# Optimization experiments

Measured on AMD Instinct MI355X. Metric: run time of the kernel, lower is better.

The kernel has to match this reference:

```python
import jax, jax.numpy as jnp
import numpy as np

LN_EPS = 1e-5  # torch.nn.LayerNorm default

QLEN, MLEN, BATCH, D_MODEL = 1024, 1024, 8, 1024


def _ft_matrix(qlen, klen):
    """Real part of the causal Fourier matrix (imag part never contributes:
    the input is real and the module takes .real of the product)."""
    ft_len = klen - qlen + 1
    m = jnp.arange(qlen, dtype=jnp.float32)
    k = jnp.arange(ft_len, dtype=jnp.float32)
    base = jnp.cos((2.0 * float(np.pi)) * jnp.outer(m, k) / float(ft_len))
    base = base / float(np.sqrt(ft_len))                      # [qlen, ft_len]
    mat = jnp.pad(base, ((0, 0), (klen - ft_len, 0)))          # left-pad -> [qlen, klen]
    # row i rolled left by (qlen - 1 - i), vectorized as a gather
    shift = (qlen - 1) - jnp.arange(qlen)                      # [qlen]
    cols = (jnp.arange(klen)[None, :] + shift[:, None]) % klen  # [qlen, klen]
    mat = jnp.take_along_axis(mat, cols, axis=1)
    rows = jnp.arange(qlen)[:, None]
    js = jnp.arange(klen)[None, :]
    # tril(diagonal=klen-qlen) AND triu(0)  (same_length=True)
    mask = (js <= rows + (klen - qlen)) & (js >= rows)
    return jnp.where(mask, mat, jnp.float32(0.0))


def setup_inputs() -> dict:
    key = jax.random.key(0)
    k1, k2, k3 = jax.random.split(key, 3)
    return {
        "dec_inp": jax.random.normal(k1, (QLEN, BATCH, D_MODEL), dtype=jnp.float32),
        "pos_emb": jax.random.normal(k2, (QLEN + MLEN, 1, D_MODEL), dtype=jnp.float32),
        "mems": jax.random.normal(k3, (MLEN, BATCH, D_MODEL), dtype=jnp.float32),
        "gamma": jnp.ones((D_MODEL,), dtype=jnp.float32),
        "beta": jnp.zeros((D_MODEL,), dtype=jnp.float32),
        "add_position": 1,
    }


def reference(dec_inp, pos_emb, mems, gamma, beta, add_position):
    qlen = dec_inp.shape[0]
    klen = qlen + mems.shape[0]
    cat = jnp.concatenate([mems, dec_inp], axis=0)  # [klen, b, d]
    if add_position:
        cat = cat + pos_emb  # dropout is identity in eval mode
    ft_mat = _ft_matrix(qlen, klen)                 # [qlen, klen]
    ft = jnp.einsum('ml,lbd->mbd', ft_mat, cat)     # real part of complex matmul
    x = dec_inp + ft / float(np.sqrt(klen))
    mu = jnp.mean(x, axis=-1, keepdims=True)
    var = jnp.var(x, axis=-1, keepdims=True)
    return gamma * (x - mu) * jax.lax.rsqrt(var + LN_EPS) + beta
```

## Files before the change

kernel.cpp:

```cpp
#include <hip/hip_runtime.h>
#include <hip/hip_bf16.h>

#define QLEN   1024
#define MLEN   1024
#define KLEN   2048
#define BATCH  8
#define DMODEL 1024
#define NCOLS  (BATCH * DMODEL)
#define FTLEN  1025

#define BM 128
#define BN 256
#define BK 64
#define NT 18

typedef __attribute__((ext_vector_type(4))) float f32x4;
typedef __attribute__((ext_vector_type(8))) short bf16x8;

typedef __attribute__((address_space(1))) const unsigned int as1_u32;
typedef __attribute__((address_space(3))) unsigned int as3_u32;

static __device__ __forceinline__ unsigned short f2bf(float f) {
    unsigned int u = __builtin_bit_cast(unsigned int, f);
    return (unsigned short)((u + 0x7fffu + ((u >> 16) & 1u)) >> 16);
}
static __device__ __forceinline__ float bf2f(unsigned short s) {
    return __builtin_bit_cast(float, (unsigned int)s << 16);
}

__global__ __launch_bounds__(256) void prep_transpose(
    const float* __restrict__ dec, const float* __restrict__ pos,
    const float* __restrict__ mems, const int* __restrict__ addp,
    unsigned short* __restrict__ catT)
{
    __shared__ unsigned short T[64][72];
    const int lt = blockIdx.x, dt = blockIdx.y, b = blockIdx.z;
    const int tid = threadIdx.x;
    const int add_position = addp[0];
    const int l0 = lt * 64, d0 = dt * 64;

    const int lrow = tid >> 4;
    const int dcol = (tid & 15) * 4;
    for (int p = 0; p < 4; ++p) {
        const int ll = p * 16 + lrow;
        const int l = l0 + ll;
        const int d = d0 + dcol;
        const float* src = (l < MLEN)
            ? (mems + (size_t)l * NCOLS + b * DMODEL + d)
            : (dec + (size_t)(l - MLEN) * NCOLS + b * DMODEL + d);
        float4 v = *reinterpret_cast<const float4*>(src);
        if (add_position) {
            float4 pv = *reinterpret_cast<const float4*>(pos + (size_t)l * DMODEL + d);
            v.x += pv.x; v.y += pv.y; v.z += pv.z; v.w += pv.w;
        }
        T[dcol + 0][ll] = f2bf(v.x);
        T[dcol + 1][ll] = f2bf(v.y);
        T[dcol + 2][ll] = f2bf(v.z);
        T[dcol + 3][ll] = f2bf(v.w);
    }
    __syncthreads();
    for (int p = 0; p < 2; ++p) {
        const int idx = p * 256 + tid;
        const int r = idx >> 3;
        const int c = (idx & 7) * 8;
        int4 v = *reinterpret_cast<const int4*>(&T[r][c]);
        size_t n = (size_t)(b * DMODEL + d0 + r);
        *reinterpret_cast<int4*>(&catT[n * KLEN + l0 + c]) = v;
    }
}

__global__ __launch_bounds__(256) void fill_w(unsigned short* __restrict__ W)
{
    const int idx = blockIdx.x * 256 + threadIdx.x;
    const int m = idx >> 9;
    const int k4 = (idx & 511) * 4;
    union { unsigned short s[4]; int2 v; } u;
    for (int j = 0; j < 4; ++j) {
        const int k = k4 + j;
        const int t = k - m;
        float w = 0.0f;
        if (t >= 0 && t < FTLEN) {
            const int r = (m * t) % FTLEN;
            const float theta = (6.283185307179586f / (float)FTLEN) * (float)r;
            w = cosf(theta) * 0.03123475237772121f;
        }
        u.s[j] = f2bf(w);
    }
    *reinterpret_cast<int2*>(&W[(size_t)m * KLEN + k4]) = u.v;
}

__global__ __launch_bounds__(512) void gemm_band3(
    const unsigned short* __restrict__ W,
    const unsigned short* __restrict__ catT,
    unsigned short* __restrict__ ftout)
{
    __shared__ unsigned short Alds[3][BM * BK];
    __shared__ unsigned short Blds[3][BN * BK];

    const int tid = threadIdx.x;
    const int wave = tid >> 6, lane = tid & 63;

    const int bid = blockIdx.x;
    const int xcd = bid & 7;
    const int kk = bid >> 3;
    const int m_idx = kk >> 2;
    const int n_idx = xcd * 4 + (kk & 3);
    const int m0 = m_idx * BM, n0 = n_idx * BN;
    const int wm = wave >> 2, wn = wave & 3;

    f32x4 acc[4][4];
    for (int i = 0; i < 4; ++i)
        for (int j = 0; j < 4; ++j)
            acc[i][j] = (f32x4){0.f, 0.f, 0.f, 0.f};

    const int srow = tid >> 3;
    const int scol = (((tid & 7) ^ ((tid >> 3) & 7)) * 8);
    const int fr = lane & 15;
    const int kg = lane >> 4;
    const int rswz = (fr & 7) * 8;

#define STAGE(S, T) do {                                                        \
    const int k0_ = m0 + (T) * BK;                                              \
    _Pragma("unroll")                                                           \
    for (int p = 0; p < 2; ++p) {                                               \
        const int row = p * 64 + srow;                                          \
        __builtin_amdgcn_global_load_lds(                                       \
            (as1_u32*)(const void*)(W + (size_t)(m0 + row) * KLEN + k0_ + scol),\
            (as3_u32*)(void*)(&Alds[S][row * BK + scol]), 16, 0, 0);            \
    }                                                                           \
    _Pragma("unroll")                                                           \
    for (int p = 0; p < 4; ++p) {                                               \
        const int row = p * 64 + srow;                                          \
        __builtin_amdgcn_global_load_lds(                                       \
            (as1_u32*)(const void*)(catT + (size_t)(n0 + row) * KLEN + k0_ + scol),\
            (as3_u32*)(void*)(&Blds[S][row * BK + scol]), 16, 0, 0);            \
    }                                                                           \
} while (0)

    STAGE(0, 0);
    STAGE(1, 1);

    for (int t = 0; t < NT; ++t) {
        if (t == NT - 1)
            asm volatile("s_waitcnt vmcnt(0)\ns_barrier" ::: "memory");
        else
            asm volatile("s_waitcnt vmcnt(6)\ns_barrier" ::: "memory");

        if (t + 2 < NT) {
            const int s = (t + 2) % 3;
            STAGE(s, t + 2);
        }

        const unsigned short* Ab = Alds[t % 3];
        const unsigned short* Bb = Blds[t % 3];
        bf16x8 a[2][4], b[2][4];
#pragma unroll
        for (int ks = 0; ks < 2; ++ks) {
#pragma unroll
            for (int f = 0; f < 4; ++f)
                a[ks][f] = *reinterpret_cast<const bf16x8*>(
                    Ab + (wm * 64 + f * 16 + fr) * BK + ((ks * 32 + kg * 8) ^ rswz));
#pragma unroll
            for (int f = 0; f < 4; ++f)
                b[ks][f] = *reinterpret_cast<const bf16x8*>(
                    Bb + (wn * 64 + f * 16 + fr) * BK + ((ks * 32 + kg * 8) ^ rswz));
        }
        __builtin_amdgcn_s_setprio(1);
#pragma unroll
        for (int ks = 0; ks < 2; ++ks)
#pragma unroll
            for (int fm = 0; fm < 4; ++fm)
#pragma unroll
                for (int fn = 0; fn < 4; ++fn)
                    acc[fm][fn] = __builtin_amdgcn_mfma_f32_16x16x32_bf16(
                        a[ks][fm], b[ks][fn], acc[fm][fn], 0, 0, 0);
        __builtin_amdgcn_s_setprio(0);
    }
#undef STAGE

    const int col16 = lane & 15, rquad = lane >> 4;
#pragma unroll
    for (int fm = 0; fm < 4; ++fm)
#pragma unroll
        for (int fn = 0; fn < 4; ++fn)
#pragma unroll
            for (int j = 0; j < 4; ++j) {
                const int m = m0 + wm * 64 + fm * 16 + rquad * 4 + j;
                const int n = n0 + wn * 64 + fn * 16 + col16;
                ftout[(size_t)m * NCOLS + n] = f2bf(acc[fm][fn][j]);
            }
}

__global__ __launch_bounds__(256) void layernorm_rows(
    const unsigned short* __restrict__ ft, const float* __restrict__ dec,
    const float* __restrict__ gamma, const float* __restrict__ beta,
    float* __restrict__ out)
{
    __shared__ float ps[4], pq[4];
    const int row = blockIdx.x;
    const int tid = threadIdx.x;
    const float inv = 0.022097086912079612f;
    const size_t base = (size_t)row * DMODEL + tid * 4;
    ushort4 u = *reinterpret_cast<const ushort4*>(ft + base);
    float4 dv = *reinterpret_cast<const float4*>(dec + base);
    float vx = dv.x + bf2f(u.x) * inv;
    float vy = dv.y + bf2f(u.y) * inv;
    float vz = dv.z + bf2f(u.z) * inv;
    float vw = dv.w + bf2f(u.w) * inv;
    float s  = vx + vy + vz + vw;
    float sq = vx * vx + vy * vy + vz * vz + vw * vw;
    for (int off = 32; off > 0; off >>= 1) {
        s  += __shfl_down(s, off);
        sq += __shfl_down(sq, off);
    }
    const int wave = tid >> 6, lane = tid & 63;
    if (lane == 0) { ps[wave] = s; pq[wave] = sq; }
    __syncthreads();
    if (tid == 0) {
        float ts = ps[0] + ps[1] + ps[2] + ps[3];
        float tq = pq[0] + pq[1] + pq[2] + pq[3];
        float mu = ts * (1.0f / DMODEL);
        float var = tq * (1.0f / DMODEL) - mu * mu;
        ps[0] = mu;
        pq[0] = rsqrtf(var + 1e-5f);
    }
    __syncthreads();
    const float mu = ps[0], rs = pq[0];
    float4 g  = *reinterpret_cast<const float4*>(gamma + tid * 4);
    float4 be = *reinterpret_cast<const float4*>(beta + tid * 4);
    float4 o;
    o.x = g.x * (vx - mu) * rs + be.x;
    o.y = g.y * (vy - mu) * rs + be.y;
    o.z = g.z * (vz - mu) * rs + be.z;
    o.w = g.w * (vw - mu) * rs + be.w;
    *reinterpret_cast<float4*>(out + base) = o;
}

extern "C" void kernel_launch(void* const* d_in, const int* in_sizes, int n_in,
                              void* d_out, int out_size, void* d_ws, size_t ws_size,
                              hipStream_t stream)
{
    const float* dec   = (const float*)d_in[0];
    const float* pos   = (const float*)d_in[1];
    const float* mems  = (const float*)d_in[2];
    const float* gamma = (const float*)d_in[3];
    const float* beta  = (const float*)d_in[4];
    const int*   addp  = (const int*)d_in[5];
    float* out = (float*)d_out;

    unsigned short* catT = (unsigned short*)d_ws;
    unsigned short* Wmat = catT + (size_t)NCOLS * KLEN;
    unsigned short* ft   = Wmat + (size_t)QLEN * KLEN;

    prep_transpose<<<dim3(32, 16, 8), 256, 0, stream>>>(dec, pos, mems, addp, catT);
    fill_w<<<2048, 256, 0, stream>>>(Wmat);
    gemm_band3<<<256, 512, 0, stream>>>(Wmat, catT, ft);
    layernorm_rows<<<8192, 256, 0, stream>>>(ft, dec, gamma, beta, out);
}
```

Measured before the change: 69.69 us.

## Split GEMM K-step into two phases interleaving prefetch with MFMA; use hardware cos

The GEMM main loop is split into two half-K phases. Each phase loads its own LDS fragments, issues half of the next-stage global-to-LDS prefetch and then runs its MFMAs, with extra barriers and lgkmcnt waits between phases so memory traffic is spread across compute. Separately, the weight-fill kernel replaces cosf with the hardware v_cos_f32 instruction on a normalized angle (input in revolutions), dropping the libm range reduction. The added barriers may cost more than the overlap gains, and the hardware cosine is a little less accurate, which bf16 rounding of the weights should absorb.

```diff
diff --git a/kernel.cpp b/kernel.cpp
--- a/kernel.cpp
+++ b/kernel.cpp
@@ -81,15 +81,17 @@
         float w = 0.0f;
         if (t >= 0 && t < FTLEN) {
             const int r = (m * t) % FTLEN;
-            const float theta = (6.283185307179586f / (float)FTLEN) * (float)r;
-            w = cosf(theta) * 0.03123475237772121f;
+            const float x = (float)r * (1.0f / (float)FTLEN);
+            float c;
+            asm("v_cos_f32 %0, %1" : "=v"(c) : "v"(x));
+            w = c * 0.03123475237772121f;
         }
         u.s[j] = f2bf(w);
     }
     *reinterpret_cast<int2*>(&W[(size_t)m * KLEN + k4]) = u.v;
 }
 
-__global__ __launch_bounds__(512) void gemm_band3(
+__global__ __launch_bounds__(512) void gemm_band4(
     const unsigned short* __restrict__ W,
     const unsigned short* __restrict__ catT,
     unsigned short* __restrict__ ftout)
@@ -119,64 +121,90 @@
     const int kg = lane >> 4;
     const int rswz = (fr & 7) * 8;
 
-#define STAGE(S, T) do {                                                        \
+#define STAGE_LOAD_A(S, T, P) do {                                              \
     const int k0_ = m0 + (T) * BK;                                              \
-    _Pragma("unroll")                                                           \
-    for (int p = 0; p < 2; ++p) {                                               \
-        const int row = p * 64 + srow;                                          \
-        __builtin_amdgcn_global_load_lds(                                       \
-            (as1_u32*)(const void*)(W + (size_t)(m0 + row) * KLEN + k0_ + scol),\
-            (as3_u32*)(void*)(&Alds[S][row * BK + scol]), 16, 0, 0);            \
-    }                                                                           \
-    _Pragma("unroll")                                                           \
-    for (int p = 0; p < 4; ++p) {                                               \
-        const int row = p * 64 + srow;                                          \
-        __builtin_amdgcn_global_load_lds(                                       \
-            (as1_u32*)(const void*)(catT + (size_t)(n0 + row) * KLEN + k0_ + scol),\
-            (as3_u32*)(void*)(&Blds[S][row * BK + scol]), 16, 0, 0);            \
-    }                                                                           \
+    const int row = (P) * 64 + srow;                                            \
+    __builtin_amdgcn_global_load_lds(                                           \
+        (as1_u32*)(const void*)(W + (size_t)(m0 + row) * KLEN + k0_ + scol),    \
+        (as3_u32*)(void*)(&Alds[S][row * BK + scol]), 16, 0, 0);                \
 } while (0)
-
-    STAGE(0, 0);
-    STAGE(1, 1);
+#define STAGE_LOAD_B(S, T, P) do {                                              \
+    const int k0_ = m0 + (T) * BK;                                              \
+    const int row = (P) * 64 + srow;                                            \
+    __builtin_amdgcn_global_load_lds(                                           \
+        (as1_u32*)(const void*)(catT + (size_t)(n0 + row) * KLEN + k0_ + scol), \
+        (as3_u32*)(void*)(&Blds[S][row * BK + scol]), 16, 0, 0);                \
+} while (0)
+#define STAGE_ALL(S, T) do {                                                    \
+    STAGE_LOAD_A(S, T, 0); STAGE_LOAD_A(S, T, 1);                               \
+    STAGE_LOAD_B(S, T, 0); STAGE_LOAD_B(S, T, 1);                               \
+    STAGE_LOAD_B(S, T, 2); STAGE_LOAD_B(S, T, 3);                               \
+} while (0)
+
+    STAGE_ALL(0, 0);
+    STAGE_ALL(1, 1);
 
     for (int t = 0; t < NT; ++t) {
         if (t == NT - 1)
-            asm volatile("s_waitcnt vmcnt(0)\ns_barrier" ::: "memory");
+            asm volatile("s_waitcnt vmcnt(0)" ::: "memory");
         else
-            asm volatile("s_waitcnt vmcnt(6)\ns_barrier" ::: "memory");
-
-        if (t + 2 < NT) {
-            const int s = (t + 2) % 3;
-            STAGE(s, t + 2);
-        }
+            asm volatile("s_waitcnt vmcnt(6)" ::: "memory");
+        __builtin_amdgcn_s_barrier();
 
         const unsigned short* Ab = Alds[t % 3];
         const unsigned short* Bb = Blds[t % 3];
-        bf16x8 a[2][4], b[2][4];
-#pragma unroll
-        for (int ks = 0; ks < 2; ++ks) {
-#pragma unroll
-            for (int f = 0; f < 4; ++f)
-                a[ks][f] = *reinterpret_cast<const bf16x8*>(
-                    Ab + (wm * 64 + f * 16 + fr) * BK + ((ks * 32 + kg * 8) ^ rswz));
-#pragma unroll
-            for (int f = 0; f < 4; ++f)
-                b[ks][f] = *reinterpret_cast<const bf16x8*>(
-                    Bb + (wn * 64 + f * 16 + fr) * BK + ((ks * 32 + kg * 8) ^ rswz));
-        }
-        __builtin_amdgcn_s_setprio(1);
-#pragma unroll
-        for (int ks = 0; ks < 2; ++ks)
+        const int s2 = (t + 2) % 3;
+        const bool pf = (t + 2 < NT);
+
+        {
+            bf16x8 a[4], b[4];
+#pragma unroll
+            for (int f = 0; f < 4; ++f)
+                a[f] = *reinterpret_cast<const bf16x8*>(
+                    Ab + (wm * 64 + f * 16 + fr) * BK + ((kg * 8) ^ rswz));
+#pragma unroll
+            for (int f = 0; f < 4; ++f)
+                b[f] = *reinterpret_cast<const bf16x8*>(
+                    Bb + (wn * 64 + f * 16 + fr) * BK + ((kg * 8) ^ rswz));
+            if (pf) { STAGE_LOAD_A(s2, t + 2, 0); STAGE_LOAD_B(s2, t + 2, 0); STAGE_LOAD_B(s2, t + 2, 1); }
+            __builtin_amdgcn_s_barrier();
+            asm volatile("s_waitcnt lgkmcnt(0)" ::: "memory");
+            __builtin_amdgcn_s_setprio(1);
 #pragma unroll
             for (int fm = 0; fm < 4; ++fm)
 #pragma unroll
                 for (int fn = 0; fn < 4; ++fn)
                     acc[fm][fn] = __builtin_amdgcn_mfma_f32_16x16x32_bf16(
-                        a[ks][fm], b[ks][fn], acc[fm][fn], 0, 0, 0);
-        __builtin_amdgcn_s_setprio(0);
-    }
-#undef STAGE
+                        a[fm], b[fn], acc[fm][fn], 0, 0, 0);
+            __builtin_amdgcn_s_setprio(0);
+            __builtin_amdgcn_s_barrier();
+        }
+        {
+            bf16x8 a[4], b[4];
+#pragma unroll
+            for (int f = 0; f < 4; ++f)
+                a[f] = *reinterpret_cast<const bf16x8*>(
+                    Ab + (wm * 64 + f * 16 + fr) * BK + ((32 + kg * 8) ^ rswz));
+#pragma unroll
+            for (int f = 0; f < 4; ++f)
+                b[f] = *reinterpret_cast<const bf16x8*>(
+                    Bb + (wn * 64 + f * 16 + fr) * BK + ((32 + kg * 8) ^ rswz));
+            if (pf) { STAGE_LOAD_A(s2, t + 2, 1); STAGE_LOAD_B(s2, t + 2, 2); STAGE_LOAD_B(s2, t + 2, 3); }
+            __builtin_amdgcn_s_barrier();
+            asm volatile("s_waitcnt lgkmcnt(0)" ::: "memory");
+            __builtin_amdgcn_s_setprio(1);
+#pragma unroll
+            for (int fm = 0; fm < 4; ++fm)
+#pragma unroll
+                for (int fn = 0; fn < 4; ++fn)
+                    acc[fm][fn] = __builtin_amdgcn_mfma_f32_16x16x32_bf16(
+                        a[fm], b[fn], acc[fm][fn], 0, 0, 0);
+            __builtin_amdgcn_s_setprio(0);
+        }
+    }
+#undef STAGE_ALL
+#undef STAGE_LOAD_A
+#undef STAGE_LOAD_B
 
     const int col16 = lane & 15, rquad = lane >> 4;
 #pragma unroll
@@ -254,6 +282,6 @@
 
     prep_transpose<<<dim3(32, 16, 8), 256, 0, stream>>>(dec, pos, mems, addp, catT);
     fill_w<<<2048, 256, 0, stream>>>(Wmat);
-    gemm_band3<<<256, 512, 0, stream>>>(Wmat, catT, ft);
+    gemm_band4<<<256, 512, 0, stream>>>(Wmat, catT, ft);
     layernorm_rows<<<8192, 256, 0, stream>>>(ft, dec, gamma, beta, out);
 }
```

Measured after the change: 64.73 us. 7.1% less time.
